# Kernel tuning notes

Hardware: AMD Instinct MI355X
Metric: run time of the kernel (lower is better)

## Reference

```python
import jax, jax.numpy as jnp
import numpy as np
from jax import lax

# Model dims (see init_kwargs / mamba_ssm defaults)
B_, L_, D_IN = 8, 512, 128
D_MODEL, N_LAYERS = 512, 2
EXPAND, D_STATE, D_CONV = 2, 16, 4
D_INNER = EXPAND * D_MODEL          # 1024
DT_RANK = (D_MODEL + 15) // 16      # 32


def setup_inputs() -> dict:
    key = jax.random.key(0)
    ks = iter(jax.random.split(key, 32))
    def p(shape, scale=0.02):
        return jax.random.normal(next(ks), shape, jnp.float32) * scale
    inp = {}
    inp["x"] = jax.random.normal(next(ks), (B_, L_, D_IN), jnp.float32)
    # input projection (Linear(input_dim, d_model), with bias)
    inp["proj_in_w"] = p((D_MODEL, D_IN))
    inp["proj_in_b"] = p((D_MODEL,))
    # stacked per-layer Mamba params (leading dim = N_LAYERS)
    inp["in_proj_w"] = p((N_LAYERS, 2 * D_INNER, D_MODEL))      # no bias (mamba default)
    inp["conv_w"]    = p((N_LAYERS, D_INNER, D_CONV))           # depthwise conv1d
    inp["conv_b"]    = p((N_LAYERS, D_INNER))
    inp["x_proj_w"]  = p((N_LAYERS, DT_RANK + 2 * D_STATE, D_INNER))
    inp["dt_proj_w"] = p((N_LAYERS, D_INNER, DT_RANK))
    inp["dt_proj_b"] = jnp.full((N_LAYERS, D_INNER), 0.1, jnp.float32)
    inp["A_log"]     = jnp.log(jnp.tile(jnp.arange(1, D_STATE + 1, dtype=jnp.float32), (N_LAYERS, D_INNER, 1)))
    inp["Dm"]        = jnp.ones((N_LAYERS, D_INNER), jnp.float32)
    inp["out_proj_w"] = p((N_LAYERS, D_MODEL, D_INNER))         # no bias
    # classifier head: Linear(d_model, 64) -> ReLU -> Linear(64, 1)
    inp["cls_w1"] = p((64, D_MODEL)); inp["cls_b1"] = p((64,))
    inp["cls_w2"] = p((1, 64));       inp["cls_b2"] = p((1,))
    return inp


def _mamba_block(h, in_w, cw, cb, xp_w, dt_w, dt_b, A_log, Dm, out_w):
    B, L, _ = h.shape
    xz = jnp.einsum('bld,ed->ble', h, in_w)           # (B, L, 2*d_inner)
    xi, z = jnp.split(xz, 2, axis=-1)
    # causal depthwise conv1d (pad left d_conv-1, crop to L)
    xc = xi.transpose(0, 2, 1)                         # (B, d_inner, L)
    xc = lax.conv_general_dilated(
        xc, cw[:, None, :], (1,), [(D_CONV - 1, 0)],
        feature_group_count=D_INNER,
        dimension_numbers=('NCH', 'OIH', 'NCH')) + cb[None, :, None]
    xc = jax.nn.silu(xc).transpose(0, 2, 1)            # (B, L, d_inner)
    x_dbl = jnp.einsum('bld,ed->ble', xc, xp_w)        # (B, L, dt_rank + 2*d_state)
    dt, Bm, Cm = jnp.split(x_dbl, [DT_RANK, DT_RANK + D_STATE], axis=-1)
    dt = jax.nn.softplus(jnp.einsum('blr,dr->bld', dt, dt_w) + dt_b)  # (B, L, d_inner)
    A = -jnp.exp(A_log)                                # (d_inner, d_state)

    def step(hst, ins):
        dt_t, B_t, C_t, x_t = ins                      # (B,di),(B,ds),(B,ds),(B,di)
        dA = jnp.exp(dt_t[..., None] * A)              # (B, di, ds)
        hst = dA * hst + (dt_t * x_t)[..., None] * B_t[:, None, :]
        y = jnp.einsum('bds,bs->bd', hst, C_t)
        return hst, y

    h0 = jnp.zeros((B, D_INNER, D_STATE), h.dtype)
    xs = (dt.transpose(1, 0, 2), Bm.transpose(1, 0, 2),
          Cm.transpose(1, 0, 2), xc.transpose(1, 0, 2))
    _, ys = lax.scan(step, h0, xs)                     # ys: (L, B, d_inner)
    y = ys.transpose(1, 0, 2) + xc * Dm                # skip term D*x
    y = y * jax.nn.silu(z)                             # gate
    return jnp.einsum('ble,de->bld', y, out_w)         # (B, L, d_model)


def reference(x, proj_in_w, proj_in_b, in_proj_w, conv_w, conv_b, x_proj_w,
              dt_proj_w, dt_proj_b, A_log, Dm, out_proj_w,
              cls_w1, cls_b1, cls_w2, cls_b2):
    h = jnp.einsum('bli,di->bld', x, proj_in_w) + proj_in_b
    for l in range(N_LAYERS):
        h = _mamba_block(h, in_proj_w[l], conv_w[l], conv_b[l], x_proj_w[l],
                         dt_proj_w[l], dt_proj_b[l], A_log[l], Dm[l], out_proj_w[l])
    h = h.mean(axis=1)                                 # (B, d_model); dropout = identity (eval)
    h = jax.nn.relu(h @ cls_w1.T + cls_b1)
    logits = (h @ cls_w2.T + cls_b2).squeeze(-1)       # (B,)
    return logits
```

## Files before the change

### kernel.cpp

```cpp
#include <hip/hip_runtime.h>
#include <hip/hip_bf16.h>

#define B_   8
#define L_   512
#define DIN  128
#define DM   512
#define NLAY 2
#define DI   1024
#define DS   16
#define DTR  32
#define BL   (B_ * L_)
#define KS   8
#define CL   128
#define NCH  (L_ / CL)

typedef short bf16x8 __attribute__((ext_vector_type(8)));
typedef float floatx4 __attribute__((ext_vector_type(4)));

__device__ __forceinline__ unsigned short f2bf(float f) {
    unsigned int u = __float_as_uint(f);
    unsigned int r = (u + 0x7FFF + ((u >> 16) & 1)) >> 16;
    return (unsigned short)r;
}
__device__ __forceinline__ float bf2f(unsigned short u) {
    return __uint_as_float((unsigned int)u << 16);
}

#if __has_builtin(__builtin_amdgcn_exp2f)
#define EXP2(x) __builtin_amdgcn_exp2f(x)
#else
#define EXP2(x) __expf((x) * 0.69314718056f)
#endif

__global__ __launch_bounds__(256) void cvt_all(
    const float* __restrict__ x,  unsigned short* __restrict__ xbf,
    const float* __restrict__ pw, unsigned short* __restrict__ wpin,
    const float* __restrict__ iw, unsigned short* __restrict__ win,
    const float* __restrict__ ow, unsigned short* __restrict__ wout)
{
    int bid = blockIdx.x;
    const float* src; unsigned short* dst; int off;
    if      (bid < 256)  { src = x;  dst = xbf;  off = bid; }
    else if (bid < 288)  { src = pw; dst = wpin; off = bid - 256; }
    else if (bid < 1312) { src = iw; dst = win;  off = bid - 288; }
    else                 { src = ow; dst = wout; off = bid - 1312; }
    int i = (off * 256 + threadIdx.x) * 8;
    float4 a = *(const float4*)(src + i);
    float4 b = *(const float4*)(src + i + 4);
    unsigned short o[8];
    o[0] = f2bf(a.x); o[1] = f2bf(a.y); o[2] = f2bf(a.z); o[3] = f2bf(a.w);
    o[4] = f2bf(b.x); o[5] = f2bf(b.y); o[6] = f2bf(b.z); o[7] = f2bf(b.w);
    *(uint4*)(dst + i) = *(uint4*)o;
}

__global__ __launch_bounds__(256) void gemm_mfma(
    const unsigned short* __restrict__ A,
    const unsigned short* __restrict__ W,
    float* __restrict__ C, unsigned short* __restrict__ Cb,
    int N, int K)
{
    __shared__ unsigned short As[128 * 40];
    __shared__ unsigned short Ws[128 * 40];

    const int tid  = threadIdx.x;
    const int row  = tid >> 1;
    const int half = tid & 1;
    const long aBase = (long)(blockIdx.y * 128 + row) * K + half * 16;
    const long wBase = (long)(blockIdx.x * 128 + row) * K + half * 16;
    const int  lbase = row * 40 + half * 16;

    const int lane = tid & 63;
    const int wv   = tid >> 6;
    const int wm   = (wv >> 1) * 64;
    const int wn   = (wv & 1) * 64;
    const int lr   = lane & 15;
    const int q    = lane >> 4;

    floatx4 acc[4][4];
#pragma unroll
    for (int i = 0; i < 4; ++i)
#pragma unroll
        for (int j = 0; j < 4; ++j)
#pragma unroll
            for (int r = 0; r < 4; ++r) acc[i][j][r] = 0.f;

    for (int k0 = 0; k0 < K; k0 += 32) {
        __syncthreads();
        const unsigned short* ap = A + aBase + k0;
        const unsigned short* wp = W + wBase + k0;
        uint4 a0 = *(const uint4*)ap;
        uint4 a1 = *(const uint4*)(ap + 8);
        uint4 w0 = *(const uint4*)wp;
        uint4 w1 = *(const uint4*)(wp + 8);
        *(uint4*)(As + lbase)     = a0;
        *(uint4*)(As + lbase + 8) = a1;
        *(uint4*)(Ws + lbase)     = w0;
        *(uint4*)(Ws + lbase + 8) = w1;
        __syncthreads();

        bf16x8 af[4], bfr[4];
#pragma unroll
        for (int i = 0; i < 4; ++i)
            af[i] = *(const bf16x8*)(As + (wm + i * 16 + lr) * 40 + q * 8);
#pragma unroll
        for (int j = 0; j < 4; ++j)
            bfr[j] = *(const bf16x8*)(Ws + (wn + j * 16 + lr) * 40 + q * 8);
#pragma unroll
        for (int i = 0; i < 4; ++i)
#pragma unroll
            for (int j = 0; j < 4; ++j)
                acc[i][j] = __builtin_amdgcn_mfma_f32_16x16x32_bf16(
                    af[i], bfr[j], acc[i][j], 0, 0, 0);
    }

#pragma unroll
    for (int i = 0; i < 4; ++i) {
#pragma unroll
        for (int r = 0; r < 4; ++r) {
            const int  crow = blockIdx.y * 128 + wm + i * 16 + q * 4 + r;
            const long base = (long)crow * N + blockIdx.x * 128 + wn + lr;
#pragma unroll
            for (int j = 0; j < 4; ++j) {
                float v = acc[i][j][r];
                if (C)  C[base + j * 16] = v;
                if (Cb) Cb[base + j * 16] = f2bf(v);
            }
        }
    }
}

__global__ __launch_bounds__(256) void gemm_mfma_n64(
    const unsigned short* __restrict__ A,
    const unsigned short* __restrict__ W,
    const float* __restrict__ bias,
    float* __restrict__ C, unsigned short* __restrict__ Cb,
    int N, int K)
{
    __shared__ unsigned short As[128 * 40];
    __shared__ unsigned short Ws[64 * 40];

    const int tid   = threadIdx.x;
    const int arow  = tid >> 1;
    const int ahalf = tid & 1;
    const long aBase = (long)(blockIdx.y * 128 + arow) * K + ahalf * 16;
    const int  albase = arow * 40 + ahalf * 16;
    const int wrow = tid >> 2;
    const int wq   = tid & 3;
    const long wBase = (long)(blockIdx.x * 64 + wrow) * K + wq * 8;
    const int  wlbase = wrow * 40 + wq * 8;

    const int lane = tid & 63;
    const int wv   = tid >> 6;
    const int wm   = wv * 32;
    const int lr   = lane & 15;
    const int q    = lane >> 4;

    floatx4 acc[2][4];
#pragma unroll
    for (int i = 0; i < 2; ++i)
#pragma unroll
        for (int j = 0; j < 4; ++j)
#pragma unroll
            for (int r = 0; r < 4; ++r) acc[i][j][r] = 0.f;

    for (int k0 = 0; k0 < K; k0 += 32) {
        __syncthreads();
        const unsigned short* ap = A + aBase + k0;
        uint4 a0 = *(const uint4*)ap;
        uint4 a1 = *(const uint4*)(ap + 8);
        uint4 w0 = *(const uint4*)(W + wBase + k0);
        *(uint4*)(As + albase)     = a0;
        *(uint4*)(As + albase + 8) = a1;
        *(uint4*)(Ws + wlbase)     = w0;
        __syncthreads();

        bf16x8 af[2], bfr[4];
#pragma unroll
        for (int i = 0; i < 2; ++i)
            af[i] = *(const bf16x8*)(As + (wm + i * 16 + lr) * 40 + q * 8);
#pragma unroll
        for (int j = 0; j < 4; ++j)
            bfr[j] = *(const bf16x8*)(Ws + (j * 16 + lr) * 40 + q * 8);
#pragma unroll
        for (int i = 0; i < 2; ++i)
#pragma unroll
            for (int j = 0; j < 4; ++j)
                acc[i][j] = __builtin_amdgcn_mfma_f32_16x16x32_bf16(
                    af[i], bfr[j], acc[i][j], 0, 0, 0);
    }

    float bj[4] = {0.f, 0.f, 0.f, 0.f};
    if (bias) {
#pragma unroll
        for (int j = 0; j < 4; ++j)
            bj[j] = bias[blockIdx.x * 64 + j * 16 + lr];
    }
#pragma unroll
    for (int i = 0; i < 2; ++i) {
#pragma unroll
        for (int r = 0; r < 4; ++r) {
            const int  crow = blockIdx.y * 128 + wm + i * 16 + q * 4 + r;
            const long base = (long)crow * N + blockIdx.x * 64 + lr;
#pragma unroll
            for (int j = 0; j < 4; ++j) {
                float v = acc[i][j][r] + bj[j];
                if (C)  C[base + j * 16] = v;
                if (Cb) Cb[base + j * 16] = f2bf(v);
            }
        }
    }
}

__global__ __launch_bounds__(256) void xprojconv(
    const unsigned short* __restrict__ xzb, const float* __restrict__ cw,
    const float* __restrict__ cb, const float* __restrict__ W,
    float* __restrict__ P, float* __restrict__ xcout)
{
    __shared__ float As[16][68];
    __shared__ float Ws[16][68];

    const int tid  = threadIdx.x;
    const int tx   = tid & 15;
    const int ty   = tid >> 4;
    const int lrow = tid >> 2;
    const int lk   = (tid & 3) << 2;
    const int kbase = blockIdx.x * (DI / KS);

    const int m = blockIdx.y * 64 + lrow;
    const int t = m & (L_ - 1);
    const float* Wp = W + lrow * DI + kbase + lk;

    float acc[4][4] = {};

    for (int k0 = 0; k0 < DI / KS; k0 += 16) {
        const int dcol = kbase + k0 + lk;
        float4 cbv = *(const float4*)(cb + dcol);
        float sums[4] = {cbv.x, cbv.y, cbv.z, cbv.w};
        float4 cwq[4];
#pragma unroll
        for (int q = 0; q < 4; ++q) cwq[q] = *(const float4*)(cw + (dcol + q) * 4);
#pragma unroll
        for (int w = 0; w < 4; ++w) {
            int tw = t - 3 + w;
            if (tw >= 0) {
                const uint2 up = *(const uint2*)(xzb + (long)(m - 3 + w) * (2 * DI) + dcol);
                float x0 = __uint_as_float(up.x << 16);
                float x1 = __uint_as_float(up.x & 0xffff0000u);
                float x2 = __uint_as_float(up.y << 16);
                float x3 = __uint_as_float(up.y & 0xffff0000u);
                sums[0] += ((const float*)&cwq[0])[w] * x0;
                sums[1] += ((const float*)&cwq[1])[w] * x1;
                sums[2] += ((const float*)&cwq[2])[w] * x2;
                sums[3] += ((const float*)&cwq[3])[w] * x3;
            }
        }
        float4 a4;
#pragma unroll
        for (int q = 0; q < 4; ++q)
            ((float*)&a4)[q] = sums[q] / (1.f + __expf(-sums[q]));
        float4 wv = *(const float4*)(Wp + k0);
        *(float4*)(xcout + (long)m * DI + dcol) = a4;

        __syncthreads();
        As[lk + 0][lrow] = a4.x; As[lk + 1][lrow] = a4.y;
        As[lk + 2][lrow] = a4.z; As[lk + 3][lrow] = a4.w;
        Ws[lk + 0][lrow] = wv.x; Ws[lk + 1][lrow] = wv.y;
        Ws[lk + 2][lrow] = wv.z; Ws[lk + 3][lrow] = wv.w;
        __syncthreads();
#pragma unroll
        for (int k = 0; k < 16; ++k) {
            const float4 a44 = *(const float4*)&As[k][ty << 2];
            const float4 w4  = *(const float4*)&Ws[k][tx << 2];
            acc[0][0] += a44.x * w4.x; acc[0][1] += a44.x * w4.y;
            acc[0][2] += a44.x * w4.z; acc[0][3] += a44.x * w4.w;
            acc[1][0] += a44.y * w4.x; acc[1][1] += a44.y * w4.y;
            acc[1][2] += a44.y * w4.z; acc[1][3] += a44.y * w4.w;
            acc[2][0] += a44.z * w4.x; acc[2][1] += a44.z * w4.y;
            acc[2][2] += a44.z * w4.z; acc[2][3] += a44.z * w4.w;
            acc[3][0] += a44.w * w4.x; acc[3][1] += a44.w * w4.y;
            acc[3][2] += a44.w * w4.z; acc[3][3] += a44.w * w4.w;
        }
    }

    float* out = P + (long)blockIdx.x * (BL * 64)
               + (blockIdx.y * 64 + (ty << 2)) * 64 + (tx << 2);
#pragma unroll
    for (int i = 0; i < 4; ++i)
        *(float4*)(out + i * 64) = make_float4(acc[i][0], acc[i][1],
                                               acc[i][2], acc[i][3]);
}

__global__ __launch_bounds__(256) void xproj_reduce(
    const float* __restrict__ P, float* __restrict__ xdbl)
{
    int i = (blockIdx.x * 256 + threadIdx.x) * 4;
    float4 s = *(const float4*)(P + i);
#pragma unroll
    for (int k = 1; k < KS; ++k) {
        float4 p = *(const float4*)(P + (long)k * (BL * 64) + i);
        s.x += p.x; s.y += p.y; s.z += p.z; s.w += p.w;
    }
    *(float4*)(xdbl + i) = s;
}

template <int CTRL>
__device__ __forceinline__ float dpp_shr_add(float v) {
    int sh = __builtin_amdgcn_update_dpp(0, __float_as_int(v), CTRL, 0xF, 0xF, true);
    return v + __int_as_float(sh);
}

__global__ __launch_bounds__(256) void scan_fused(
    const float* __restrict__ xc, const float* __restrict__ xdbl,
    const float* __restrict__ A_log, const float* __restrict__ dtw,
    const float* __restrict__ dtpb, const float* __restrict__ Dm,
    const unsigned short* __restrict__ xzb, unsigned short* __restrict__ ysb16)
{
    __shared__ float  sdtw[16][36];
    __shared__ float  sxd [CL][36];
    __shared__ float4 sdp [CL / 2][17];
    __shared__ float4 sbc4[CL / 2][17];
    __shared__ float  sy  [16][CL + 4];

    const int tid  = threadIdx.x;
    const int s    = tid & 15;
    const int grp  = tid >> 4;
    const int bd0  = blockIdx.x * 16;
    const int b    = bd0 >> 10;
    const int d0   = bd0 & (DI - 1);
    const int mb0  = b * L_;

    const int j  = tid & 15;
    const int tt = tid >> 4;

    {
        float2 w = *(const float2*)(dtw + (d0 + j) * DTR + tt * 2);
        sdtw[j][tt * 2] = w.x; sdtw[j][tt * 2 + 1] = w.y;
    }
    const float a    = -__expf(A_log[(d0 + grp) * DS + s]);
    const float bias = dtpb[d0 + j];
    const float dmv  = Dm[d0 + j];

    float  rxc[8], rB[8], rC[8], rz[8];
    float2 rxd[8];
#pragma unroll
    for (int i = 0; i < 8; ++i) {
        int m = mb0 + tt + 16 * i;
        rxc[i] = xc[m * DI + d0 + j];
        rxd[i] = *(const float2*)(xdbl + m * 64 + j * 2);
        rB[i]  = xdbl[m * 64 + DTR + j];
        rC[i]  = xdbl[m * 64 + DTR + DS + j];
        rz[i]  = bf2f(xzb[(long)m * (2 * DI) + DI + d0 + j]);
    }

    float state = 0.f;

    for (int c = 0; c < NCH; ++c) {
        const int mbase = mb0 + c * CL;
        float xcur[8], zcur[8];
#pragma unroll
        for (int i = 0; i < 8; ++i) { xcur[i] = rxc[i]; zcur[i] = rz[i]; }

        __syncthreads();
#pragma unroll
        for (int i = 0; i < 8; ++i) {
            int t = tt + 16 * i;
            *(float2*)&sxd[t][j * 2] = rxd[i];
            ((float2*)&sbc4[t >> 1][j])[t & 1] = make_float2(rB[i], rC[i]);
        }
        __syncthreads();

        if (c < NCH - 1) {
#pragma unroll
            for (int i = 0; i < 8; ++i) {
                int m = mbase + CL + tt + 16 * i;
                rxc[i] = xc[m * DI + d0 + j];
                rxd[i] = *(const float2*)(xdbl + m * 64 + j * 2);
                rB[i]  = xdbl[m * 64 + DTR + j];
                rC[i]  = xdbl[m * 64 + DTR + DS + j];
                rz[i]  = bf2f(xzb[(long)m * (2 * DI) + DI + d0 + j]);
            }
        }

        {
            float4 wreg[8];
#pragma unroll
            for (int k = 0; k < 8; ++k) wreg[k] = *(const float4*)&sdtw[j][k * 4];
#pragma unroll
            for (int i = 0; i < 8; ++i) {
                int t = tt + 16 * i;
                float acc = bias;
#pragma unroll
                for (int k = 0; k < 8; ++k) {
                    float4 xv = *(const float4*)&sxd[t][k * 4];
                    acc += xv.x * wreg[k].x + xv.y * wreg[k].y
                         + xv.z * wreg[k].z + xv.w * wreg[k].w;
                }
                float dt = (acc > 20.f) ? acc : __logf(1.f + __expf(acc));
                ((float2*)&sdp[t >> 1][j])[t & 1] =
                    make_float2(dt * 1.44269504f, dt * xcur[i]);
            }
        }
        __syncthreads();

        for (int t4 = 0; t4 < CL; t4 += 4) {
            float ybuf[4];
#pragma unroll
            for (int h = 0; h < 2; ++h) {
                const int t2 = (t4 >> 1) + h;
                const float4 dp = sdp[t2][grp];
                const float4 bc = sbc4[t2][s];
                {
                    const float dA = EXP2(dp.x * a);
                    state = fmaf(dA, state, dp.y * bc.x);
                    float contrib = state * bc.y;
                    contrib = dpp_shr_add<0x111>(contrib);
                    contrib = dpp_shr_add<0x112>(contrib);
                    contrib = dpp_shr_add<0x114>(contrib);
                    contrib = dpp_shr_add<0x118>(contrib);
                    ybuf[h * 2] = contrib;
                }
                {
                    const float dA = EXP2(dp.z * a);
                    state = fmaf(dA, state, dp.w * bc.z);
                    float contrib = state * bc.w;
                    contrib = dpp_shr_add<0x111>(contrib);
                    contrib = dpp_shr_add<0x112>(contrib);
                    contrib = dpp_shr_add<0x114>(contrib);
                    contrib = dpp_shr_add<0x118>(contrib);
                    ybuf[h * 2 + 1] = contrib;
                }
            }
            if (s == 15) *(float4*)&sy[grp][t4] = *(float4*)ybuf;
        }
        __syncthreads();

#pragma unroll
        for (int i = 0; i < 8; ++i) {
            int t = tt + 16 * i;
            float z = zcur[i];
            float sz = z / (1.f + __expf(-z));
            float val = (sy[j][t] + xcur[i] * dmv) * sz;
            ysb16[(mbase + t) * DI + d0 + j] = f2bf(val);
        }
    }
}

__global__ __launch_bounds__(512) void mean_partial(
    const float* __restrict__ h, float* __restrict__ hmp)
{
    int b = blockIdx.x >> 3, sl = blockIdx.x & 7, d = threadIdx.x;
    float acc = 0.f;
    int t0 = sl * 64;
    for (int t = 0; t < 64; ++t) acc += h[(b * L_ + t0 + t) * DM + d];
    hmp[blockIdx.x * DM + d] = acc;
}

__global__ __launch_bounds__(512) void meancls_kernel(
    const float* __restrict__ hmp, const float* __restrict__ w1,
    const float* __restrict__ b1, const float* __restrict__ w2,
    const float* __restrict__ b2, float* __restrict__ out)
{
    __shared__ float shm[DM];
    __shared__ float su[64];
    const int b = blockIdx.x, tid = threadIdx.x;
    float acc = 0.f;
#pragma unroll
    for (int sl = 0; sl < 8; ++sl) acc += hmp[(b * 8 + sl) * DM + tid];
    shm[tid] = acc * (1.f / (float)L_);
    __syncthreads();

    const int j = tid >> 3, sl = tid & 7;
    const float* wr = w1 + j * DM + sl * 64;
    const float* hb = shm + sl * 64;
    float p = 0.f;
    for (int k = 0; k < 64; k += 4)
        p += hb[k] * wr[k] + hb[k+1] * wr[k+1]
           + hb[k+2] * wr[k+2] + hb[k+3] * wr[k+3];
    p += __shfl_xor(p, 1);
    p += __shfl_xor(p, 2);
    p += __shfl_xor(p, 4);
    if (sl == 0) su[j] = fmaxf(p + b1[j], 0.f) * w2[j];
    __syncthreads();
    if (tid < 64) {
        float v = su[tid];
#pragma unroll
        for (int off = 32; off; off >>= 1) v += __shfl_down(v, off);
        if (tid == 0) out[b] = v + b2[0];
    }
}

extern "C" void kernel_launch(void* const* d_in, const int* in_sizes, int n_in,
                              void* d_out, int out_size, void* d_ws, size_t ws_size,
                              hipStream_t stream) {
    const float* x          = (const float*)d_in[0];
    const float* proj_in_w  = (const float*)d_in[1];
    const float* proj_in_b  = (const float*)d_in[2];
    const float* in_proj_w  = (const float*)d_in[3];
    const float* conv_w     = (const float*)d_in[4];
    const float* conv_b     = (const float*)d_in[5];
    const float* x_proj_w   = (const float*)d_in[6];
    const float* dt_proj_w  = (const float*)d_in[7];
    const float* dt_proj_b  = (const float*)d_in[8];
    const float* A_log      = (const float*)d_in[9];
    const float* Dm         = (const float*)d_in[10];
    const float* out_proj_w = (const float*)d_in[11];
    const float* cls_w1     = (const float*)d_in[12];
    const float* cls_b1     = (const float*)d_in[13];
    const float* cls_w2     = (const float*)d_in[14];
    const float* cls_b2     = (const float*)d_in[15];
    float* out = (float*)d_out;

    float* ws   = (float*)d_ws;
    float* h    = ws;
    float* xzf  = h    + BL * DM;
    float* xcb  = xzf  + BL * 2 * DI;
    float* xdbl = xcb  + BL * DI;
    float* scr  = xdbl + BL * 64;
    float* hm   = scr  + 2 * BL * DI;
    float* hmp  = hm   + B_ * DM;
    unsigned short* xzb  = (unsigned short*)xzf;
    unsigned short* u16  = (unsigned short*)(hmp + 64 * DM);
    unsigned short* xbf  = u16;
    unsigned short* hbf  = xbf  + BL * DIN;
    unsigned short* ysbf = hbf  + BL * DM;
    unsigned short* wpin = ysbf + BL * DI;
    unsigned short* win  = wpin + DM * DIN;
    unsigned short* wout = win  + NLAY * 2 * DI * DM;
    float* xpart = scr;

    cvt_all<<<1824, 256, 0, stream>>>(x, xbf, proj_in_w, wpin,
                                      in_proj_w, win, out_proj_w, wout);

    gemm_mfma_n64<<<dim3(DM / 64, BL / 128), 256, 0, stream>>>(
        xbf, wpin, proj_in_b, h, hbf, DM, DIN);

    for (int l = 0; l < NLAY; ++l) {
        gemm_mfma<<<dim3(2 * DI / 128, BL / 128), 256, 0, stream>>>(
            hbf, win + l * 2 * DI * DM, nullptr, xzb, 2 * DI, DM);
        xprojconv<<<dim3(KS, BL / 64), 256, 0, stream>>>(
            xzb, conv_w + l * DI * 4, conv_b + l * DI,
            x_proj_w + l * 64 * DI, xpart, xcb);
        xproj_reduce<<<(BL * 64) / 1024, 256, 0, stream>>>(xpart, xdbl);
        scan_fused<<<(B_ * DI) / 16, 256, 0, stream>>>(
            xcb, xdbl, A_log + l * DI * DS, dt_proj_w + l * DI * DTR,
            dt_proj_b + l * DI, Dm + l * DI, xzb, ysbf);
        gemm_mfma_n64<<<dim3(DM / 64, BL / 128), 256, 0, stream>>>(
            ysbf, wout + l * DM * DI, nullptr, h, hbf, DM, DI);
    }

    mean_partial<<<B_ * 8, DM, 0, stream>>>(h, hmp);
    meancls_kernel<<<B_, 512, 0, stream>>>(hmp, cls_w1, cls_b1,
                                           cls_w2, cls_b2, out);
}
```

Before: 351.3 us.

## Fuse split-K reduction via atomics and mean-pool into output GEMM epilogue

Drops the xproj_reduce kernel by having each split-K block of xprojconv atomically add its partial results into a pre-zeroed xdbl buffer, and drops the mean_partial kernel by reducing the last out_proj GEMM's tile columns in shared memory and atomically adding the scaled sums into hm. The zeroing work is folded into cvt_all and, for later layers, into the in_proj GEMM. It also stops writing the fp32 h buffer that nothing reads anymore. This removes two launches plus the partial-buffer and h traffic, at the cost of global float atomics and a summation order that is no longer deterministic.

```diff
diff --git a/kernel.cpp b/kernel.cpp
--- a/kernel.cpp
+++ b/kernel.cpp
@@ -36,9 +36,23 @@
     const float* __restrict__ x,  unsigned short* __restrict__ xbf,
     const float* __restrict__ pw, unsigned short* __restrict__ wpin,
     const float* __restrict__ iw, unsigned short* __restrict__ win,
-    const float* __restrict__ ow, unsigned short* __restrict__ wout)
+    const float* __restrict__ ow, unsigned short* __restrict__ wout,
+    float* __restrict__ xdbl, float* __restrict__ hm)
 {
     int bid = blockIdx.x;
+    if (bid >= 1824) {
+        float4 z = make_float4(0.f, 0.f, 0.f, 0.f);
+        if (bid < 1952) {
+            int i = (bid - 1824) * 2048 + threadIdx.x * 8;
+            *(float4*)(xdbl + i) = z;
+            *(float4*)(xdbl + i + 4) = z;
+        } else {
+            int i = (bid - 1952) * 2048 + threadIdx.x * 8;
+            *(float4*)(hm + i) = z;
+            *(float4*)(hm + i + 4) = z;
+        }
+        return;
+    }
     const float* src; unsigned short* dst; int off;
     if      (bid < 256)  { src = x;  dst = xbf;  off = bid; }
     else if (bid < 288)  { src = pw; dst = wpin; off = bid - 256; }
@@ -57,12 +71,22 @@
     const unsigned short* __restrict__ A,
     const unsigned short* __restrict__ W,
     float* __restrict__ C, unsigned short* __restrict__ Cb,
-    int N, int K)
+    int N, int K, float* __restrict__ zbuf)
 {
     __shared__ unsigned short As[128 * 40];
     __shared__ unsigned short Ws[128 * 40];
 
     const int tid  = threadIdx.x;
+    if (zbuf) {
+        int flat = blockIdx.y * gridDim.x + blockIdx.x;
+        if (flat < 128) {
+            int i = flat * 2048 + tid * 8;
+            float4 z = make_float4(0.f, 0.f, 0.f, 0.f);
+            *(float4*)(zbuf + i) = z;
+            *(float4*)(zbuf + i + 4) = z;
+        }
+    }
+
     const int row  = tid >> 1;
     const int half = tid & 1;
     const long aBase = (long)(blockIdx.y * 128 + row) * K + half * 16;
@@ -134,10 +158,11 @@
     const unsigned short* __restrict__ W,
     const float* __restrict__ bias,
     float* __restrict__ C, unsigned short* __restrict__ Cb,
-    int N, int K)
+    int N, int K, int meanmode, float* __restrict__ hm)
 {
     __shared__ unsigned short As[128 * 40];
     __shared__ unsigned short Ws[64 * 40];
+    __shared__ float colsum[64];
 
     const int tid   = threadIdx.x;
     const int arow  = tid >> 1;
@@ -189,6 +214,27 @@
                     af[i], bfr[j], acc[i][j], 0, 0, 0);
     }
 
+    if (meanmode) {
+        if (tid < 64) colsum[tid] = 0.f;
+        __syncthreads();
+#pragma unroll
+        for (int j = 0; j < 4; ++j) {
+            float p = 0.f;
+#pragma unroll
+            for (int i = 0; i < 2; ++i)
+#pragma unroll
+                for (int r = 0; r < 4; ++r) p += acc[i][j][r];
+            atomicAdd(&colsum[j * 16 + lr], p);
+        }
+        __syncthreads();
+        if (tid < 64) {
+            const int b = blockIdx.y >> 2;
+            atomicAdd(&hm[b * DM + blockIdx.x * 64 + tid],
+                      colsum[tid] * (1.f / (float)L_));
+        }
+        return;
+    }
+
     float bj[4] = {0.f, 0.f, 0.f, 0.f};
     if (bias) {
 #pragma unroll
@@ -214,7 +260,7 @@
 __global__ __launch_bounds__(256) void xprojconv(
     const unsigned short* __restrict__ xzb, const float* __restrict__ cw,
     const float* __restrict__ cb, const float* __restrict__ W,
-    float* __restrict__ P, float* __restrict__ xcout)
+    float* __restrict__ xdbl, float* __restrict__ xcout)
 {
     __shared__ float As[16][68];
     __shared__ float Ws[16][68];
@@ -282,25 +328,12 @@
         }
     }
 
-    float* out = P + (long)blockIdx.x * (BL * 64)
-               + (blockIdx.y * 64 + (ty << 2)) * 64 + (tx << 2);
+    float* xrow = xdbl + (blockIdx.y * 64 + (ty << 2)) * 64 + (tx << 2);
 #pragma unroll
     for (int i = 0; i < 4; ++i)
-        *(float4*)(out + i * 64) = make_float4(acc[i][0], acc[i][1],
-                                               acc[i][2], acc[i][3]);
-}
-
-__global__ __launch_bounds__(256) void xproj_reduce(
-    const float* __restrict__ P, float* __restrict__ xdbl)
-{
-    int i = (blockIdx.x * 256 + threadIdx.x) * 4;
-    float4 s = *(const float4*)(P + i);
-#pragma unroll
-    for (int k = 1; k < KS; ++k) {
-        float4 p = *(const float4*)(P + (long)k * (BL * 64) + i);
-        s.x += p.x; s.y += p.y; s.z += p.z; s.w += p.w;
-    }
-    *(float4*)(xdbl + i) = s;
+#pragma unroll
+        for (int q = 0; q < 4; ++q)
+            atomicAdd(&xrow[i * 64 + q], acc[i][q]);
 }
 
 template <int CTRL>
@@ -445,28 +478,15 @@
     }
 }
 
-__global__ __launch_bounds__(512) void mean_partial(
-    const float* __restrict__ h, float* __restrict__ hmp)
-{
-    int b = blockIdx.x >> 3, sl = blockIdx.x & 7, d = threadIdx.x;
-    float acc = 0.f;
-    int t0 = sl * 64;
-    for (int t = 0; t < 64; ++t) acc += h[(b * L_ + t0 + t) * DM + d];
-    hmp[blockIdx.x * DM + d] = acc;
-}
-
 __global__ __launch_bounds__(512) void meancls_kernel(
-    const float* __restrict__ hmp, const float* __restrict__ w1,
+    const float* __restrict__ hm, const float* __restrict__ w1,
     const float* __restrict__ b1, const float* __restrict__ w2,
     const float* __restrict__ b2, float* __restrict__ out)
 {
     __shared__ float shm[DM];
     __shared__ float su[64];
     const int b = blockIdx.x, tid = threadIdx.x;
-    float acc = 0.f;
-#pragma unroll
-    for (int sl = 0; sl < 8; ++sl) acc += hmp[(b * 8 + sl) * DM + tid];
-    shm[tid] = acc * (1.f / (float)L_);
+    shm[tid] = hm[b * DM + tid];
     __syncthreads();
 
     const int j = tid >> 3, sl = tid & 7;
@@ -526,29 +546,35 @@
     unsigned short* wpin = ysbf + BL * DI;
     unsigned short* win  = wpin + DM * DIN;
     unsigned short* wout = win  + NLAY * 2 * DI * DM;
-    float* xpart = scr;
-
-    cvt_all<<<1824, 256, 0, stream>>>(x, xbf, proj_in_w, wpin,
-                                      in_proj_w, win, out_proj_w, wout);
+
+    cvt_all<<<1954, 256, 0, stream>>>(x, xbf, proj_in_w, wpin,
+                                      in_proj_w, win, out_proj_w, wout,
+                                      xdbl, hm);
 
     gemm_mfma_n64<<<dim3(DM / 64, BL / 128), 256, 0, stream>>>(
-        xbf, wpin, proj_in_b, h, hbf, DM, DIN);
+        xbf, wpin, proj_in_b, nullptr, hbf, DM, DIN, 0, nullptr);
 
     for (int l = 0; l < NLAY; ++l) {
         gemm_mfma<<<dim3(2 * DI / 128, BL / 128), 256, 0, stream>>>(
-            hbf, win + l * 2 * DI * DM, nullptr, xzb, 2 * DI, DM);
+            hbf, win + l * 2 * DI * DM, nullptr, xzb, 2 * DI, DM,
+            (l > 0) ? xdbl : nullptr);
         xprojconv<<<dim3(KS, BL / 64), 256, 0, stream>>>(
             xzb, conv_w + l * DI * 4, conv_b + l * DI,
-            x_proj_w + l * 64 * DI, xpart, xcb);
-        xproj_reduce<<<(BL * 64) / 1024, 256, 0, stream>>>(xpart, xdbl);
+            x_proj_w + l * 64 * DI, xdbl, xcb);
         scan_fused<<<(B_ * DI) / 16, 256, 0, stream>>>(
             xcb, xdbl, A_log + l * DI * DS, dt_proj_w + l * DI * DTR,
             dt_proj_b + l * DI, Dm + l * DI, xzb, ysbf);
-        gemm_mfma_n64<<<dim3(DM / 64, BL / 128), 256, 0, stream>>>(
-            ysbf, wout + l * DM * DI, nullptr, h, hbf, DM, DI);
-    }
-
-    mean_partial<<<B_ * 8, DM, 0, stream>>>(h, hmp);
-    meancls_kernel<<<B_, 512, 0, stream>>>(hmp, cls_w1, cls_b1,
+        if (l == NLAY - 1) {
+            gemm_mfma_n64<<<dim3(DM / 64, BL / 128), 256, 0, stream>>>(
+                ysbf, wout + l * DM * DI, nullptr, nullptr, nullptr,
+                DM, DI, 1, hm);
+        } else {
+            gemm_mfma_n64<<<dim3(DM / 64, BL / 128), 256, 0, stream>>>(
+                ysbf, wout + l * DM * DI, nullptr, nullptr, hbf,
+                DM, DI, 0, nullptr);
+        }
+    }
+
+    meancls_kernel<<<B_, 512, 0, stream>>>(hm, cls_w1, cls_b1,
                                            cls_w2, cls_b2, out);
 }
```

Result: slower. 387.9 us (+10.4%).
